# Kernel optimization log

Measured on AMD Instinct MI355X. Metric: run time of the kernel, lower is better.

The kernel has to match this reference:

```python
import jax, jax.numpy as jnp
import numpy as np

L, N, D = 4, 65536, 512
NUM_HEADS = 4
LN_EPS = 1e-5
NEG_INF = -1e30


def setup_inputs() -> dict:
    key = jax.random.key(0)
    ks = jax.random.split(key, 8)
    s = 0.02
    x = jax.random.normal(ks[0], (L, N, D), dtype=jnp.float32)
    Wq = jax.random.normal(ks[1], (L, D, D), dtype=jnp.float32) * s
    Wk = jax.random.normal(ks[2], (L, D, D), dtype=jnp.float32) * s
    Wv = jax.random.normal(ks[3], (L, D, D), dtype=jnp.float32) * s
    W1 = jax.random.normal(ks[4], (L, D, D), dtype=jnp.float32) * s
    W2 = jax.random.normal(ks[5], (L, D, D), dtype=jnp.float32) * s
    bq = jnp.zeros((L, D), jnp.float32)
    bk = jnp.zeros((L, D), jnp.float32)
    bv = jnp.zeros((L, D), jnp.float32)
    b1 = jnp.zeros((L, D), jnp.float32)
    b2 = jnp.zeros((L, D), jnp.float32)
    gamma = jnp.ones((L, D), jnp.float32)
    beta = jnp.zeros((L, D), jnp.float32)
    return dict(x=x, Wq=Wq, bq=bq, Wk=Wk, bk=bk, Wv=Wv, bv=bv,
                W1=W1, b1=b1, W2=W2, b2=b2, gamma=gamma, beta=beta)


def reference(x, Wq, bq, Wk, bk, Wv, bv, W1, b1, W2, b2, gamma, beta):
    # x: (L, N, D) per-level node features
    scale = (D // NUM_HEADS) ** -0.5
    summ = x.mean(axis=1)  # (L, D) per-level pooled summary
    # per-level Q/K/V projections (each level has its own weights)
    q = jnp.einsum('ld,lde->le', summ, Wq) + bq
    k = jnp.einsum('ld,lde->le', summ, Wk) + bk
    v = jnp.einsum('ld,lde->le', summ, Wv) + bv
    # each target level attends to summaries of all OTHER levels
    scores = (q @ k.T) * scale                      # (L, L)
    scores = jnp.where(jnp.eye(L, dtype=bool), NEG_INF, scores)
    attn = jax.nn.softmax(scores, axis=-1)          # dropout is identity in eval
    ctx = attn @ v                                  # (L, D)
    # per-level output MLP: Linear -> ReLU -> Linear
    h = jax.nn.relu(jnp.einsum('ld,lde->le', ctx, W1) + b1)
    upd = jnp.einsum('ld,lde->le', h, W2) + b2      # (L, D)
    # gated residual update broadcast to all nodes, then LayerNorm
    y = x + upd[:, None, :]                         # (L, N, D)
    mu = y.mean(axis=-1, keepdims=True)
    var = y.var(axis=-1, keepdims=True)
    out = (y - mu) * jax.lax.rsqrt(var + LN_EPS) * gamma[:, None, :] + beta[:, None, :]
    return out
```

## Files before the change

### kernel.cpp

```cpp
#include <hip/hip_runtime.h>
#include <math.h>

#define LVL 4
#define NN 65536
#define DD 512
#define NBLK 256
#define ROWS_PER_BLK (NN / NBLK)
#define LN_EPS 1e-5f
#define ATTN_SCALE 0.08838834764831845f

typedef float f32x4 __attribute__((ext_vector_type(4)));

#define WS_PARTIALS 0
#define WS_QKV  (WS_PARTIALS + LVL*NBLK*DD)
#define WS_H    (WS_QKV + 3*LVL*DD)
#define WS_UPD  (WS_H + LVL*DD)

__device__ __forceinline__ void acc4(float4& a, const float4 v) {
    a.x += v.x; a.y += v.y; a.z += v.z; a.w += v.w;
}

__global__ __launch_bounds__(256) void colsum_kernel(const float* __restrict__ x,
                                                     float* __restrict__ partials) {
    int blk = blockIdx.x;
    int l = blk >> 8;
    int b = blk & 255;
    int t = threadIdx.x;
    int lane = t & 127;
    int rg = t >> 7;
    const float4* xp = (const float4*)(x + ((size_t)l * NN + (size_t)b * ROWS_PER_BLK) * DD);
    float4 a0 = make_float4(0.f,0.f,0.f,0.f), a1 = a0, a2 = a0, a3 = a0;
    for (int i = 0; i < 128; i += 4) {
        float4 v0 = xp[(size_t)((i + 0) * 2 + rg) * (DD / 4) + lane];
        float4 v1 = xp[(size_t)((i + 1) * 2 + rg) * (DD / 4) + lane];
        float4 v2 = xp[(size_t)((i + 2) * 2 + rg) * (DD / 4) + lane];
        float4 v3 = xp[(size_t)((i + 3) * 2 + rg) * (DD / 4) + lane];
        acc4(a0, v0); acc4(a1, v1); acc4(a2, v2); acc4(a3, v3);
    }
    acc4(a0, a1); acc4(a2, a3); acc4(a0, a2);
    __shared__ float4 red[128];
    if (rg) red[lane] = a0;
    __syncthreads();
    if (!rg) {
        acc4(a0, red[lane]);
        ((float4*)(partials + (size_t)(l * NBLK + b) * DD))[lane] = a0;
    }
}

__global__ __launch_bounds__(1024) void qkv_kernel(const float* __restrict__ partials,
                                                   const float* __restrict__ Wq,
                                                   const float* __restrict__ bq,
                                                   const float* __restrict__ Wk,
                                                   const float* __restrict__ bk,
                                                   const float* __restrict__ Wv,
                                                   const float* __restrict__ bv,
                                                   const float* __restrict__ W1,
                                                   const float* __restrict__ W2,
                                                   float* __restrict__ qkv) {
    int blk = blockIdx.x;
    int t = threadIdx.x;

    if (blk >= 96) {
        const int NF4 = LVL * DD * DD / 4;
        int idx0 = (blk - 96) * 1024 + t;
        const float4* w1 = (const float4*)W1;
        const float4* w2 = (const float4*)W2;
        float4 a = make_float4(0.f,0.f,0.f,0.f);
        for (int i = idx0; i < NF4; i += 16384) {
            acc4(a, w1[i]);
            acc4(a, w2[i]);
        }
        float keep = a.x + a.y + a.z + a.w;
        asm volatile("" :: "v"(keep));
        return;
    }

    int mat = blk >> 5;
    int sub = blk & 31;
    int l = sub >> 3, ec = sub & 7;
    const float* W    = (mat == 0) ? Wq : (mat == 1) ? Wk : Wv;
    const float* bias = (mat == 0) ? bq : (mat == 1) ? bk : bv;

    __shared__ float summ[DD];
    __shared__ float red[1024];

    {
        int d = t & 511, half = t >> 9;
        const float* p = partials + (size_t)l * NBLK * DD + d;
        float s0 = 0.f, s1 = 0.f;
        for (int b = half * 128; b < half * 128 + 128; b += 2) {
            s0 += p[(size_t)b * DD];
            s1 += p[(size_t)(b + 1) * DD];
        }
        float s = s0 + s1;
        if (half) red[d] = s;
        __syncthreads();
        if (!half) summ[d] = (s + red[d]) * (1.0f / NN);
        __syncthreads();
    }

    int e = t & 63, dg = t >> 6;
    int ecol = ec * 64 + e;
    const float* Wl = W + (size_t)l * DD * DD;
    float acc = 0.f;
    for (int d = dg * 32; d < dg * 32 + 32; ++d)
        acc += summ[d] * Wl[(size_t)d * DD + ecol];
    red[t] = acc;
    __syncthreads();
    for (int s = 512; s >= 64; s >>= 1) {
        if (t < s) red[t] += red[t + s];
        __syncthreads();
    }
    if (t < 64)
        qkv[(size_t)mat * LVL * DD + (size_t)l * DD + ec * 64 + t] =
            red[t] + bias[(size_t)l * DD + ec * 64 + t];
}

__global__ __launch_bounds__(1024) void attn_h_kernel(const float* __restrict__ qkv,
                                                      const float* __restrict__ W1,
                                                      const float* __restrict__ b1,
                                                      float* __restrict__ h) {
    int l = blockIdx.x >> 3, ec = blockIdx.x & 7;
    int t = threadIdx.x;
    const float* q = qkv;
    const float* k = qkv + LVL * DD;
    const float* v = qkv + 2 * LVL * DD;

    __shared__ float red[1024];
    __shared__ float atw[LVL];
    __shared__ float ctx[DD];

    {
        int j = t >> 8, dd = t & 255;
        float a = q[l * DD + dd] * k[j * DD + dd]
                + q[l * DD + dd + 256] * k[j * DD + dd + 256];
        red[t] = a;
        __syncthreads();
        for (int s = 128; s >= 1; s >>= 1) {
            if ((t & 255) < s) red[t] += red[t + s];
            __syncthreads();
        }
        if (t == 0) {
            float sc[LVL], m = -1e30f;
            for (int jj = 0; jj < LVL; ++jj) {
                sc[jj] = (jj == l) ? -1e30f : red[jj * 256] * ATTN_SCALE;
                m = fmaxf(m, sc[jj]);
            }
            float ssum = 0.f;
            for (int jj = 0; jj < LVL; ++jj) { sc[jj] = expf(sc[jj] - m); ssum += sc[jj]; }
            float inv = 1.0f / ssum;
            for (int jj = 0; jj < LVL; ++jj) atw[jj] = sc[jj] * inv;
        }
        __syncthreads();
    }

    if (t < DD) {
        float c = 0.f;
        for (int jj = 0; jj < LVL; ++jj) c += atw[jj] * v[jj * DD + t];
        ctx[t] = c;
    }
    __syncthreads();

    int e = t & 63, dg = t >> 6;
    int ecol = ec * 64 + e;
    const float* Wl = W1 + (size_t)l * DD * DD;
    float acc = 0.f;
    for (int d = dg * 32; d < dg * 32 + 32; ++d)
        acc += ctx[d] * Wl[(size_t)d * DD + ecol];
    red[t] = acc;
    __syncthreads();
    for (int s = 512; s >= 64; s >>= 1) {
        if (t < s) red[t] += red[t + s];
        __syncthreads();
    }
    if (t < 64) {
        float r = red[t] + b1[(size_t)l * DD + ec * 64 + t];
        h[(size_t)l * DD + ec * 64 + t] = fmaxf(r, 0.f);
    }
}

__global__ __launch_bounds__(1024) void matvec1024_kernel(const float* __restrict__ in,
                                                          const float* __restrict__ W,
                                                          const float* __restrict__ bias,
                                                          float* __restrict__ out) {
    int l = blockIdx.x >> 3, ec = blockIdx.x & 7;
    int t = threadIdx.x;
    __shared__ float red[1024];
    int e = t & 63, dg = t >> 6;
    int ecol = ec * 64 + e;
    const float* iv = in + (size_t)l * DD;
    const float* Wl = W + (size_t)l * DD * DD;
    float acc = 0.f;
    for (int d = dg * 32; d < dg * 32 + 32; ++d)
        acc += iv[d] * Wl[(size_t)d * DD + ecol];
    red[t] = acc;
    __syncthreads();
    for (int s = 512; s >= 64; s >>= 1) {
        if (t < s) red[t] += red[t + s];
        __syncthreads();
    }
    if (t < 64)
        out[(size_t)l * DD + ec * 64 + t] = red[t] + bias[(size_t)l * DD + ec * 64 + t];
}

__global__ __launch_bounds__(256) void final_ln_kernel(const float* __restrict__ x,
                                                       const float* __restrict__ upd,
                                                       const float* __restrict__ gamma,
                                                       const float* __restrict__ beta,
                                                       float* __restrict__ out) {
    int lane = threadIdx.x & 63;
    int wid = (blockIdx.x * blockDim.x + threadIdx.x) >> 6;
    const int NW = (2048 * 256) >> 6;
    const int totalRows = LVL * NN;
    int lprev = -1;
    float4 u0, u1, g0, g1, p0, p1;
    for (int it = wid; it < totalRows; it += NW) {
        int r = totalRows - 1 - it;
        int l = r >> 16;
        if (l != lprev) {
            lprev = l;
            const float4* ur = (const float4*)(upd + (size_t)l * DD);
            u0 = ur[lane]; u1 = ur[64 + lane];
            const float4* gr = (const float4*)(gamma + (size_t)l * DD);
            g0 = gr[lane]; g1 = gr[64 + lane];
            const float4* br = (const float4*)(beta + (size_t)l * DD);
            p0 = br[lane]; p1 = br[64 + lane];
        }
        const float4* xr = (const float4*)(x + (size_t)r * DD);
        float4 a = xr[lane];
        float4 c = xr[64 + lane];
        a.x += u0.x; a.y += u0.y; a.z += u0.z; a.w += u0.w;
        c.x += u1.x; c.y += u1.y; c.z += u1.z; c.w += u1.w;
        float s  = a.x + a.y + a.z + a.w + c.x + c.y + c.z + c.w;
        float sq = a.x * a.x + a.y * a.y + a.z * a.z + a.w * a.w
                 + c.x * c.x + c.y * c.y + c.z * c.z + c.w * c.w;
        for (int off = 32; off >= 1; off >>= 1) {
            s  += __shfl_down(s, off);
            sq += __shfl_down(sq, off);
        }
        s = __shfl(s, 0);
        sq = __shfl(sq, 0);
        float mu = s * (1.0f / DD);
        float var = sq * (1.0f / DD) - mu * mu;
        float inv = rsqrtf(var + LN_EPS);
        float4 o0, o1;
        o0.x = (a.x - mu) * inv * g0.x + p0.x;
        o0.y = (a.y - mu) * inv * g0.y + p0.y;
        o0.z = (a.z - mu) * inv * g0.z + p0.z;
        o0.w = (a.w - mu) * inv * g0.w + p0.w;
        o1.x = (c.x - mu) * inv * g1.x + p1.x;
        o1.y = (c.y - mu) * inv * g1.y + p1.y;
        o1.z = (c.z - mu) * inv * g1.z + p1.z;
        o1.w = (c.w - mu) * inv * g1.w + p1.w;
        float* orow = out + (size_t)r * DD;
        __builtin_nontemporal_store(*(const f32x4*)&o0, (f32x4*)(orow) + lane);
        __builtin_nontemporal_store(*(const f32x4*)&o1, (f32x4*)(orow) + 64 + lane);
    }
}

extern "C" void kernel_launch(void* const* d_in, const int* in_sizes, int n_in,
                              void* d_out, int out_size, void* d_ws, size_t ws_size,
                              hipStream_t stream) {
    const float* x     = (const float*)d_in[0];
    const float* Wq    = (const float*)d_in[1];
    const float* bq    = (const float*)d_in[2];
    const float* Wk    = (const float*)d_in[3];
    const float* bk    = (const float*)d_in[4];
    const float* Wv    = (const float*)d_in[5];
    const float* bv    = (const float*)d_in[6];
    const float* W1    = (const float*)d_in[7];
    const float* b1    = (const float*)d_in[8];
    const float* W2    = (const float*)d_in[9];
    const float* b2    = (const float*)d_in[10];
    const float* gamma = (const float*)d_in[11];
    const float* beta  = (const float*)d_in[12];
    float* out = (float*)d_out;
    float* ws = (float*)d_ws;

    float* partials = ws + WS_PARTIALS;
    float* qkv      = ws + WS_QKV;
    float* h        = ws + WS_H;
    float* upd      = ws + WS_UPD;

    colsum_kernel<<<LVL * NBLK, 256, 0, stream>>>(x, partials);
    qkv_kernel<<<112, 1024, 0, stream>>>(partials, Wq, bq, Wk, bk, Wv, bv, W1, W2, qkv);
    attn_h_kernel<<<32, 1024, 0, stream>>>(qkv, W1, b1, h);
    matvec1024_kernel<<<32, 1024, 0, stream>>>(h, W2, b2, upd);
    final_ln_kernel<<<2048, 256, 0, stream>>>(x, upd, gamma, beta, out);
}
```

Baseline: 304.9 us.

## Fuse attention, first MLP layer and second MLP layer into one kernel

Merges the attention+W1 kernel and the W2 matvec into a single kernel. Each block recomputes the full hidden vector for its level (all 512 outputs of W1) into shared memory, then computes its 64-column slice of W2. This removes one kernel launch and the global round trip for h. In exchange, each of the 8 blocks per level redundantly reads the whole W1 matrix for that level.

```diff
diff --git a/kernel.cpp b/kernel.cpp
--- a/kernel.cpp
+++ b/kernel.cpp
@@ -13,8 +13,7 @@
 
 #define WS_PARTIALS 0
 #define WS_QKV  (WS_PARTIALS + LVL*NBLK*DD)
-#define WS_H    (WS_QKV + 3*LVL*DD)
-#define WS_UPD  (WS_H + LVL*DD)
+#define WS_UPD  (WS_QKV + 3*LVL*DD)
 
 __device__ __forceinline__ void acc4(float4& a, const float4 v) {
     a.x += v.x; a.y += v.y; a.z += v.z; a.w += v.w;
@@ -116,10 +115,12 @@
             red[t] + bias[(size_t)l * DD + ec * 64 + t];
 }
 
-__global__ __launch_bounds__(1024) void attn_h_kernel(const float* __restrict__ qkv,
-                                                      const float* __restrict__ W1,
-                                                      const float* __restrict__ b1,
-                                                      float* __restrict__ h) {
+__global__ __launch_bounds__(1024) void attn_mlp_kernel(const float* __restrict__ qkv,
+                                                        const float* __restrict__ W1,
+                                                        const float* __restrict__ b1,
+                                                        const float* __restrict__ W2,
+                                                        const float* __restrict__ b2,
+                                                        float* __restrict__ upd) {
     int l = blockIdx.x >> 3, ec = blockIdx.x & 7;
     int t = threadIdx.x;
     const float* q = qkv;
@@ -129,6 +130,7 @@
     __shared__ float red[1024];
     __shared__ float atw[LVL];
     __shared__ float ctx[DD];
+    __shared__ float hsh[DD];
 
     {
         int j = t >> 8, dd = t & 255;
@@ -161,46 +163,41 @@
     }
     __syncthreads();
 
-    int e = t & 63, dg = t >> 6;
-    int ecol = ec * 64 + e;
-    const float* Wl = W1 + (size_t)l * DD * DD;
-    float acc = 0.f;
-    for (int d = dg * 32; d < dg * 32 + 32; ++d)
-        acc += ctx[d] * Wl[(size_t)d * DD + ecol];
-    red[t] = acc;
-    __syncthreads();
-    for (int s = 512; s >= 64; s >>= 1) {
-        if (t < s) red[t] += red[t + s];
-        __syncthreads();
-    }
-    if (t < 64) {
-        float r = red[t] + b1[(size_t)l * DD + ec * 64 + t];
-        h[(size_t)l * DD + ec * 64 + t] = fmaxf(r, 0.f);
-    }
-}
-
-__global__ __launch_bounds__(1024) void matvec1024_kernel(const float* __restrict__ in,
-                                                          const float* __restrict__ W,
-                                                          const float* __restrict__ bias,
-                                                          float* __restrict__ out) {
-    int l = blockIdx.x >> 3, ec = blockIdx.x & 7;
-    int t = threadIdx.x;
-    __shared__ float red[1024];
-    int e = t & 63, dg = t >> 6;
-    int ecol = ec * 64 + e;
-    const float* iv = in + (size_t)l * DD;
-    const float* Wl = W + (size_t)l * DD * DD;
-    float acc = 0.f;
-    for (int d = dg * 32; d < dg * 32 + 32; ++d)
-        acc += iv[d] * Wl[(size_t)d * DD + ecol];
-    red[t] = acc;
-    __syncthreads();
-    for (int s = 512; s >= 64; s >>= 1) {
-        if (t < s) red[t] += red[t + s];
-        __syncthreads();
-    }
-    if (t < 64)
-        out[(size_t)l * DD + ec * 64 + t] = red[t] + bias[(size_t)l * DD + ec * 64 + t];
+    {
+        int e = t & 511, dh = t >> 9;
+        const float* W1l = W1 + (size_t)l * DD * DD;
+        int dbase = dh * 256;
+        float a0 = 0.f, a1 = 0.f, a2 = 0.f, a3 = 0.f;
+        for (int d = 0; d < 256; d += 4) {
+            a0 += ctx[dbase + d]     * W1l[(size_t)(dbase + d)     * DD + e];
+            a1 += ctx[dbase + d + 1] * W1l[(size_t)(dbase + d + 1) * DD + e];
+            a2 += ctx[dbase + d + 2] * W1l[(size_t)(dbase + d + 2) * DD + e];
+            a3 += ctx[dbase + d + 3] * W1l[(size_t)(dbase + d + 3) * DD + e];
+        }
+        red[t] = (a0 + a1) + (a2 + a3);
+        __syncthreads();
+        if (t < 512)
+            hsh[t] = fmaxf(red[t] + red[t + 512] + b1[(size_t)l * DD + t], 0.f);
+        __syncthreads();
+    }
+
+    {
+        int e = t & 63, dg = t >> 6;
+        int ecol = ec * 64 + e;
+        const float* W2l = W2 + (size_t)l * DD * DD;
+        float acc = 0.f;
+        for (int d = dg * 32; d < dg * 32 + 32; ++d)
+            acc += hsh[d] * W2l[(size_t)d * DD + ecol];
+        red[t] = acc;
+        __syncthreads();
+        for (int s = 512; s >= 64; s >>= 1) {
+            if (t < s) red[t] += red[t + s];
+            __syncthreads();
+        }
+        if (t < 64)
+            upd[(size_t)l * DD + ec * 64 + t] =
+                red[t] + b2[(size_t)l * DD + ec * 64 + t];
+    }
 }
 
 __global__ __launch_bounds__(256) void final_ln_kernel(const float* __restrict__ x,
@@ -279,12 +276,10 @@
 
     float* partials = ws + WS_PARTIALS;
     float* qkv      = ws + WS_QKV;
-    float* h        = ws + WS_H;
     float* upd      = ws + WS_UPD;
 
     colsum_kernel<<<LVL * NBLK, 256, 0, stream>>>(x, partials);
     qkv_kernel<<<112, 1024, 0, stream>>>(partials, Wq, bq, Wk, bk, Wv, bv, W1, W2, qkv);
-    attn_h_kernel<<<32, 1024, 0, stream>>>(qkv, W1, b1, h);
-    matvec1024_kernel<<<32, 1024, 0, stream>>>(h, W2, b2, upd);
+    attn_mlp_kernel<<<32, 1024, 0, stream>>>(qkv, W1, b1, W2, b2, upd);
     final_ln_kernel<<<2048, 256, 0, stream>>>(x, upd, gamma, beta, out);
 }
```

After: 312.2 us. 1.02x slower.
